# Optimization experiments

Hardware: AMD Instinct MI355X
Metric: run time of the kernel (lower is better)

Reference implementation:

```python
import jax, jax.numpy as jnp
import numpy as np

ALPHA = 0.1
BETA = 0.3
MARGIN = 2.0


def setup_inputs() -> dict:
    key = jax.random.key(0)
    k1, k2 = jax.random.split(key)
    prediction = jax.random.normal(k1, (8, 2048, 512), dtype=jnp.float32)
    target_seg = jax.random.randint(k2, (8, 2048), 0, 16, dtype=jnp.int64)
    return {"prediction": prediction, "target_seg": target_seg}


def _pairwise_sqdist(x):
    # x: [n, L, d] -> squared Euclidean distances [n, L, L] via a GEMM
    sq = jnp.sum(x * x, axis=-1)  # [n, L]
    inner = jnp.einsum('nld,nmd->nlm', x, x)  # [n, L, L]
    d2 = sq[:, :, None] + sq[:, None, :] - 2.0 * inner
    return jnp.maximum(d2, 0.0)


def _safe_sqrt(d2):
    # sqrt with zero (not NaN) gradient at 0, matching torch.cdist behavior
    pos = d2 > 0
    return jnp.where(pos, jnp.sqrt(jnp.where(pos, d2, 1.0)), 0.0)


def reference(prediction, target_seg):
    # y[i,j,k] = 1 if target_seg[i,j] == target_seg[i,k]
    y = (target_seg[:, :, None] == target_seg[:, None, :]).astype(prediction.dtype)
    d2 = _pairwise_sqdist(prediction)
    dist = _safe_sqrt(d2)
    hinge = jnp.maximum(MARGIN - dist, 0.0)
    loss = ALPHA * y * d2 + BETA * (1.0 - y) * hinge * hinge
    return jnp.mean(loss)
```

## Files before the change

kernel.cpp:

```cpp
#include <hip/hip_runtime.h>
#include <math.h>

#define L      2048
#define DDIM   512
#define NBATCH 8
#define BM     128
#define BN     128
#define BK     128
#define NST    (DDIM / BK)
#define NTILE  (L / BM)
#define NPAIR  (NTILE * (NTILE + 1) / 2)
#define TOTAL_BLOCKS (NBATCH * NPAIR)

#define ALPHA  0.1f
#define BETA   0.3f
#define MARGIN 2.0f

typedef _Float16 f16x8 __attribute__((ext_vector_type(8)));
typedef __attribute__((ext_vector_type(16))) float f32x16;

#define AHALF  8192
#define BOFF   16384

#define GLOAD_LDS16(g, l) __builtin_amdgcn_global_load_lds(              \
    (const __attribute__((address_space(1))) unsigned int*)(g),          \
    (__attribute__((address_space(3))) unsigned int*)(l), 16, 0, 0)

__global__ __launch_bounds__(256) void conv_kernel(const float* __restrict__ pred,
                                                   _Float16* __restrict__ h,
                                                   float* __restrict__ sq) {
    int w     = threadIdx.x >> 6;
    int lane  = threadIdx.x & 63;
    int batch = blockIdx.x & 7;
    int idx   = blockIdx.x >> 3;
    int row   = batch * L + idx * 4 + w;
    const float* p = pred + (size_t)row * DDIM + lane * 8;
    float4 v0 = *(const float4*)(p);
    float4 v1 = *(const float4*)(p + 4);
    float vals[8] = {v0.x, v0.y, v0.z, v0.w, v1.x, v1.y, v1.z, v1.w};
    f16x8 hv;
    float s = 0.0f;
    #pragma unroll
    for (int i = 0; i < 8; ++i) {
        float x = vals[i];
        s = fmaf(x, x, s);
        hv[i] = (_Float16)x;
    }
    *(f16x8*)(h + (size_t)row * DDIM + lane * 8) = hv;
    #pragma unroll
    for (int off = 32; off > 0; off >>= 1) s += __shfl_down(s, off);
    if (lane == 0) sq[row] = s;
}

__global__ __launch_bounds__(256) void loss_kernel(
        const _Float16* __restrict__ h,
        const int*   __restrict__ seg,
        const float* __restrict__ sq,
        double*      __restrict__ partials) {
    __shared__ _Float16 smem[32768];
    __shared__ double wred[4];

    int bid = blockIdx.x;
    int n = bid & 7;
    int p = bid >> 3;
    int tj = 0;
    while (true) {
        int rl2 = NTILE - tj;
        if (p < rl2) break;
        p -= rl2;
        ++tj;
    }
    int tk = tj + p;
    int j0 = tj * BM, k0 = tk * BN;

    int t    = threadIdx.x;
    int w    = t >> 6;
    int lane = t & 63;
    int wr   = w >> 1, wc = w & 1;
    int l31  = lane & 31;
    int hsel = lane >> 5;

    const _Float16* baseH = h + (size_t)n * L * DDIM;

    int rl8 = lane >> 3;
    int lc  = (lane & 7) ^ rl8;
    const _Float16* srcA = baseH + (size_t)(j0 + w * 32 + rl8) * DDIM + lc * 8;
    const _Float16* srcB = baseH + (size_t)(k0 + w * 32 + rl8) * DDIM + lc * 8;
    _Float16* dstA = smem + w * 2048;
    _Float16* dstB = smem + BOFF + w * 2048;

    #define STAGE(st)                                                         \
    {                                                                         \
        _Pragma("unroll")                                                     \
        for (int q = 0; q < 4; ++q)                                           \
            _Pragma("unroll")                                                 \
            for (int kh = 0; kh < 2; ++kh) {                                  \
                GLOAD_LDS16(srcA + (size_t)(q * 8) * DDIM + (st) * BK + kh * 64, \
                            dstA + kh * AHALF + q * 512);                     \
                GLOAD_LDS16(srcB + (size_t)(q * 8) * DDIM + (st) * BK + kh * 64, \
                            dstB + kh * AHALF + q * 512);                     \
            }                                                                 \
    }

    int s7 = l31 & 7;
    int ra = (wr * 64 + l31) * 64;
    int rb = (wc * 64 + l31) * 64 + BOFF;
    int iA0 = ra + (((0 + hsel) ^ s7) << 3);
    int iA1 = ra + (((2 + hsel) ^ s7) << 3);
    int iA2 = ra + (((4 + hsel) ^ s7) << 3);
    int iA3 = ra + (((6 + hsel) ^ s7) << 3);
    int iB0 = rb + (((0 + hsel) ^ s7) << 3);
    int iB1 = rb + (((2 + hsel) ^ s7) << 3);
    int iB2 = rb + (((4 + hsel) ^ s7) << 3);
    int iB3 = rb + (((6 + hsel) ^ s7) << 3);

    f32x16 acc[2][2];
    #pragma unroll
    for (int m = 0; m < 2; ++m)
        #pragma unroll
        for (int nn = 0; nn < 2; ++nn)
            #pragma unroll
            for (int r = 0; r < 16; ++r) acc[m][nn][r] = 0.0f;

    #pragma unroll
    for (int st = 0; st < NST; ++st) {
        __syncthreads();
        STAGE(st);
        __syncthreads();

        #pragma unroll
        for (int ks = 0; ks < 8; ++ks) {
            int kq = ks & 3;
            int kh = ks >> 2;
            int iA = ((kq == 0) ? iA0 : (kq == 1) ? iA1 : (kq == 2) ? iA2 : iA3)
                     + kh * AHALF;
            int iB = ((kq == 0) ? iB0 : (kq == 1) ? iB1 : (kq == 2) ? iB2 : iB3)
                     + kh * AHALF;
            f16x8 a0 = *(const f16x8*)&smem[iA];
            f16x8 a1 = *(const f16x8*)&smem[iA + 2048];
            f16x8 b0 = *(const f16x8*)&smem[iB];
            f16x8 b1 = *(const f16x8*)&smem[iB + 2048];
            acc[0][0] = __builtin_amdgcn_mfma_f32_32x32x16_f16(a0, b0, acc[0][0], 0, 0, 0);
            acc[0][1] = __builtin_amdgcn_mfma_f32_32x32x16_f16(a0, b1, acc[0][1], 0, 0, 0);
            acc[1][0] = __builtin_amdgcn_mfma_f32_32x32x16_f16(a1, b0, acc[1][0], 0, 0, 0);
            acc[1][1] = __builtin_amdgcn_mfma_f32_32x32x16_f16(a1, b1, acc[1][1], 0, 0, 0);
        }
    }

    const int*   segb = seg + n * L;
    const float* sqb  = sq + n * L;

    float lsum = 0.0f;
    #pragma unroll
    for (int nn = 0; nn < 2; ++nn) {
        int k = k0 + wc * 64 + nn * 32 + l31;
        float sqk = sqb[k];
        int   sgk = segb[k];
        #pragma unroll
        for (int m = 0; m < 2; ++m)
            #pragma unroll
            for (int r = 0; r < 16; ++r) {
                int j = j0 + wr * 64 + m * 32 + (r & 3) + 8 * (r >> 2) + 4 * hsel;
                float inner = acc[m][nn][r];
                float d2 = fmaxf(sqb[j] + sqk - 2.0f * inner, 0.0f);
                float v;
                if (segb[j] == sgk) {
                    v = ALPHA * d2;
                } else {
                    float dist = sqrtf(d2);
                    float hg = fmaxf(MARGIN - dist, 0.0f);
                    v = BETA * hg * hg;
                }
                lsum += v;
            }
    }

    double wgt = (tj == tk) ? 1.0 : 2.0;
    double dsum = (double)lsum * wgt;
    #pragma unroll
    for (int off = 32; off > 0; off >>= 1)
        dsum += __shfl_down(dsum, off);
    if (lane == 0) wred[w] = dsum;
    __syncthreads();
    if (t == 0) partials[bid] = (wred[0] + wred[1]) + (wred[2] + wred[3]);
}

__global__ __launch_bounds__(256) void reduce_kernel(const double* __restrict__ partials,
                                                     float* __restrict__ out,
                                                     int nPart, double invCount) {
    __shared__ double red[256];
    int t = threadIdx.x;
    double s = 0.0;
    for (int i = t; i < nPart; i += 256) s += partials[i];
    red[t] = s;
    __syncthreads();
    #pragma unroll
    for (int k = 128; k > 0; k >>= 1) {
        if (t < k) red[t] += red[t + k];
        __syncthreads();
    }
    if (t == 0) out[0] = (float)(red[0] * invCount);
}

extern "C" void kernel_launch(void* const* d_in, const int* in_sizes, int n_in,
                              void* d_out, int out_size, void* d_ws, size_t ws_size,
                              hipStream_t stream) {
    const float* pred = (const float*)d_in[0];
    const int*   seg  = (const int*)d_in[1];
    float* out = (float*)d_out;

    const size_t HALF = (size_t)NBATCH * L * DDIM;
    _Float16* h        = (_Float16*)d_ws;
    float*    sq       = (float*)(h + HALF);
    double*   partials = (double*)(sq + NBATCH * L);

    conv_kernel<<<NBATCH * L / 4, 256, 0, stream>>>(pred, h, sq);
    loss_kernel<<<TOTAL_BLOCKS, 256, 0, stream>>>(h, seg, sq, partials);
    reduce_kernel<<<1, 256, 0, stream>>>(partials, out, TOTAL_BLOCKS,
                                         1.0 / (double)((size_t)NBATCH * L * L));
}
```

Before: 61.49 us.

## Quantize prediction to FP8 e4m3 and use FP8 MFMA for Gram matrix

The conversion kernel now writes FP8 e4m3 instead of FP16, and the loss kernel computes the inner products with the 32x32x16 FP8 MFMA instruction. The LDS layout and swizzle are rewritten for byte elements. This halves the bytes staged per K-block and uses the higher-throughput FP8 matrix path. In exchange it adds quantization error in the inner products that feed d2, which could hurt accuracy, particularly for the hinge term near the margin.

```diff
diff --git a/kernel.cpp b/kernel.cpp
--- a/kernel.cpp
+++ b/kernel.cpp
@@ -1,4 +1,5 @@
 #include <hip/hip_runtime.h>
+#include <hip/hip_fp8.h>
 #include <math.h>
 
 #define L      2048
@@ -16,10 +17,9 @@
 #define BETA   0.3f
 #define MARGIN 2.0f
 
+typedef __attribute__((ext_vector_type(16))) float f32x16;
 typedef _Float16 f16x8 __attribute__((ext_vector_type(8)));
-typedef __attribute__((ext_vector_type(16))) float f32x16;
-
-#define AHALF  8192
+
 #define BOFF   16384
 
 #define GLOAD_LDS16(g, l) __builtin_amdgcn_global_load_lds(              \
@@ -27,7 +27,7 @@
     (__attribute__((address_space(3))) unsigned int*)(l), 16, 0, 0)
 
 __global__ __launch_bounds__(256) void conv_kernel(const float* __restrict__ pred,
-                                                   _Float16* __restrict__ h,
+                                                   unsigned char* __restrict__ h,
                                                    float* __restrict__ sq) {
     int w     = threadIdx.x >> 6;
     int lane  = threadIdx.x & 63;
@@ -38,26 +38,29 @@
     float4 v0 = *(const float4*)(p);
     float4 v1 = *(const float4*)(p + 4);
     float vals[8] = {v0.x, v0.y, v0.z, v0.w, v1.x, v1.y, v1.z, v1.w};
-    f16x8 hv;
+    unsigned q[8];
     float s = 0.0f;
     #pragma unroll
     for (int i = 0; i < 8; ++i) {
         float x = vals[i];
         s = fmaf(x, x, s);
-        hv[i] = (_Float16)x;
-    }
-    *(f16x8*)(h + (size_t)row * DDIM + lane * 8) = hv;
+        __hip_fp8_e4m3 f8(x);
+        q[i] = (unsigned)f8.__x;
+    }
+    unsigned lo = q[0] | (q[1] << 8) | (q[2] << 16) | (q[3] << 24);
+    unsigned hi = q[4] | (q[5] << 8) | (q[6] << 16) | (q[7] << 24);
+    *(uint2*)(h + (size_t)row * DDIM + lane * 8) = make_uint2(lo, hi);
     #pragma unroll
     for (int off = 32; off > 0; off >>= 1) s += __shfl_down(s, off);
     if (lane == 0) sq[row] = s;
 }
 
 __global__ __launch_bounds__(256) void loss_kernel(
-        const _Float16* __restrict__ h,
+        const unsigned char* __restrict__ h,
         const int*   __restrict__ seg,
         const float* __restrict__ sq,
         double*      __restrict__ partials) {
-    __shared__ _Float16 smem[32768];
+    __shared__ unsigned char smem[32768];
     __shared__ double wred[4];
 
     int bid = blockIdx.x;
@@ -80,39 +83,29 @@
     int l31  = lane & 31;
     int hsel = lane >> 5;
 
-    const _Float16* baseH = h + (size_t)n * L * DDIM;
+    const unsigned char* baseH = h + (size_t)n * L * DDIM;
 
     int rl8 = lane >> 3;
     int lc  = (lane & 7) ^ rl8;
-    const _Float16* srcA = baseH + (size_t)(j0 + w * 32 + rl8) * DDIM + lc * 8;
-    const _Float16* srcB = baseH + (size_t)(k0 + w * 32 + rl8) * DDIM + lc * 8;
-    _Float16* dstA = smem + w * 2048;
-    _Float16* dstB = smem + BOFF + w * 2048;
+    const unsigned char* srcA = baseH + (size_t)(j0 + w * 32 + rl8) * DDIM + lc * 16;
+    const unsigned char* srcB = baseH + (size_t)(k0 + w * 32 + rl8) * DDIM + lc * 16;
+    unsigned char* dstA = smem + w * 4096;
+    unsigned char* dstB = smem + BOFF + w * 4096;
 
     #define STAGE(st)                                                         \
     {                                                                         \
         _Pragma("unroll")                                                     \
-        for (int q = 0; q < 4; ++q)                                           \
-            _Pragma("unroll")                                                 \
-            for (int kh = 0; kh < 2; ++kh) {                                  \
-                GLOAD_LDS16(srcA + (size_t)(q * 8) * DDIM + (st) * BK + kh * 64, \
-                            dstA + kh * AHALF + q * 512);                     \
-                GLOAD_LDS16(srcB + (size_t)(q * 8) * DDIM + (st) * BK + kh * 64, \
-                            dstB + kh * AHALF + q * 512);                     \
-            }                                                                 \
-    }
-
-    int s7 = l31 & 7;
-    int ra = (wr * 64 + l31) * 64;
-    int rb = (wc * 64 + l31) * 64 + BOFF;
-    int iA0 = ra + (((0 + hsel) ^ s7) << 3);
-    int iA1 = ra + (((2 + hsel) ^ s7) << 3);
-    int iA2 = ra + (((4 + hsel) ^ s7) << 3);
-    int iA3 = ra + (((6 + hsel) ^ s7) << 3);
-    int iB0 = rb + (((0 + hsel) ^ s7) << 3);
-    int iB1 = rb + (((2 + hsel) ^ s7) << 3);
-    int iB2 = rb + (((4 + hsel) ^ s7) << 3);
-    int iB3 = rb + (((6 + hsel) ^ s7) << 3);
+        for (int q = 0; q < 4; ++q) {                                         \
+            GLOAD_LDS16(srcA + (size_t)(q * 8) * DDIM + (st) * BK,            \
+                        dstA + q * 1024);                                     \
+            GLOAD_LDS16(srcB + (size_t)(q * 8) * DDIM + (st) * BK,            \
+                        dstB + q * 1024);                                     \
+        }                                                                     \
+    }
+
+    int s7  = l31 & 7;
+    int rab = (wr * 64 + l31) * 128 + hsel * 8;
+    int rbb = BOFF + (wc * 64 + l31) * 128 + hsel * 8;
 
     f32x16 acc[2][2];
     #pragma unroll
@@ -130,20 +123,15 @@
 
         #pragma unroll
         for (int ks = 0; ks < 8; ++ks) {
-            int kq = ks & 3;
-            int kh = ks >> 2;
-            int iA = ((kq == 0) ? iA0 : (kq == 1) ? iA1 : (kq == 2) ? iA2 : iA3)
-                     + kh * AHALF;
-            int iB = ((kq == 0) ? iB0 : (kq == 1) ? iB1 : (kq == 2) ? iB2 : iB3)
-                     + kh * AHALF;
-            f16x8 a0 = *(const f16x8*)&smem[iA];
-            f16x8 a1 = *(const f16x8*)&smem[iA + 2048];
-            f16x8 b0 = *(const f16x8*)&smem[iB];
-            f16x8 b1 = *(const f16x8*)&smem[iB + 2048];
-            acc[0][0] = __builtin_amdgcn_mfma_f32_32x32x16_f16(a0, b0, acc[0][0], 0, 0, 0);
-            acc[0][1] = __builtin_amdgcn_mfma_f32_32x32x16_f16(a0, b1, acc[0][1], 0, 0, 0);
-            acc[1][0] = __builtin_amdgcn_mfma_f32_32x32x16_f16(a1, b0, acc[1][0], 0, 0, 0);
-            acc[1][1] = __builtin_amdgcn_mfma_f32_32x32x16_f16(a1, b1, acc[1][1], 0, 0, 0);
+            int xo = (ks ^ s7) << 4;
+            long a0 = *(const long*)&smem[rab + xo];
+            long a1 = *(const long*)&smem[rab + 4096 + xo];
+            long b0 = *(const long*)&smem[rbb + xo];
+            long b1 = *(const long*)&smem[rbb + 4096 + xo];
+            acc[0][0] = __builtin_amdgcn_mfma_f32_32x32x16_fp8_fp8(a0, b0, acc[0][0], 0, 0, 0);
+            acc[0][1] = __builtin_amdgcn_mfma_f32_32x32x16_fp8_fp8(a0, b1, acc[0][1], 0, 0, 0);
+            acc[1][0] = __builtin_amdgcn_mfma_f32_32x32x16_fp8_fp8(a1, b0, acc[1][0], 0, 0, 0);
+            acc[1][1] = __builtin_amdgcn_mfma_f32_32x32x16_fp8_fp8(a1, b1, acc[1][1], 0, 0, 0);
         }
     }
 
@@ -210,9 +198,9 @@
     float* out = (float*)d_out;
 
     const size_t HALF = (size_t)NBATCH * L * DDIM;
-    _Float16* h        = (_Float16*)d_ws;
-    float*    sq       = (float*)(h + HALF);
-    double*   partials = (double*)(sq + NBATCH * L);
+    unsigned char* h  = (unsigned char*)d_ws;
+    float*  sq        = (float*)(h + HALF);
+    double* partials  = (double*)(sq + NBATCH * L);
 
     conv_kernel<<<NBATCH * L / 4, 256, 0, stream>>>(pred, h, sq);
     loss_kernel<<<TOTAL_BLOCKS, 256, 0, stream>>>(h, seg, sq, partials);
```

Result: faster. 55.84 us (-9.2%).
